# Kernel tuning notes

Measured on AMD Instinct MI355X. Metric: run time of the kernel, lower is better.

## Reference

```python
import jax, jax.numpy as jnp
import numpy as np

T, B, D, H, O = 128, 256, 512, 1024, 20
THR = 1.0
ALPHA = float(np.exp(-1.0 / 20.0))  # exp(-dt/tau_m)
KAPPA = float(np.exp(-1.0 / 20.0))  # exp(-dt/tau_o)
B_O = 0.0


def setup_inputs() -> dict:
    key = jax.random.key(0)
    k1, k2, k3, k4 = jax.random.split(key, 4)
    x = jax.random.normal(k1, (T, B, D), dtype=jnp.float32)
    # kaiming_normal: std = sqrt(2/fan_in), gain = 1.0
    w_in = jax.random.normal(k2, (H, D), dtype=jnp.float32) * np.sqrt(2.0 / D)
    w_rec = jax.random.normal(k3, (H, H), dtype=jnp.float32) * np.sqrt(2.0 / H)
    w_out = jax.random.normal(k4, (O, H), dtype=jnp.float32) * np.sqrt(2.0 / H)
    return {"x": x, "w_in": w_in, "w_rec": w_rec, "w_out": w_out}


def reference(x, w_in, w_rec, w_out):
    # mask out self-recurrence (diagonal zeroed)
    w_rec_eff = w_rec * (1.0 - jnp.eye(w_rec.shape[0], dtype=w_rec.dtype))

    def step(carry, x_t):
        v, z, vo = carry
        v_new = ALPHA * v + z @ w_rec_eff.T + x_t @ w_in.T - z * THR
        z_new = (v_new > THR).astype(v_new.dtype)
        vo_new = KAPPA * vo + z_new @ w_out.T + B_O
        return (v_new, z_new, vo_new), vo_new

    v0 = jnp.zeros((x.shape[1], w_rec.shape[0]), dtype=x.dtype)
    vo0 = jnp.zeros((x.shape[1], w_out.shape[0]), dtype=x.dtype)
    # torch loop runs t = 0..T-2, consuming x[0..T-2]; vo[0] stays zero
    _, vo_rest = jax.lax.scan(step, (v0, v0, vo0), x[:-1])
    vo = jnp.concatenate([vo0[None], vo_rest], axis=0)  # [T, B, O]
    return jax.nn.softmax(vo, axis=2)
```

## Files before the change

kernel.cpp:

```cpp
#include <hip/hip_runtime.h>
#include <math.h>


#define T_ 128
#define B_ 256
#define D_ 512
#define H_ 1024
#define O_ 20
#define ST_ 127
#define WPB 32
#define ALPHA_F ((float)0.95122942450071400909)
#define KAPPA_F ((float)0.95122942450071400909)

typedef float v2f __attribute__((ext_vector_type(2)));

#if defined(__has_builtin)
#if __has_builtin(__builtin_elementwise_fma)
#define PK_FMA(a, b, c) __builtin_elementwise_fma(a, b, c)
#endif
#if __has_builtin(__builtin_amdgcn_global_load_lds)
#define HAVE_GLL 1
#endif
#endif
#ifndef PK_FMA
static __device__ inline v2f pk_fma_impl(v2f a, v2f b, v2f c) {
    v2f r; r[0] = __fmaf_rn(a[0], b[0], c[0]); r[1] = __fmaf_rn(a[1], b[1], c[1]);
    return r;
}
#define PK_FMA(a, b, c) pk_fma_impl(a, b, c)
#endif

static __device__ __forceinline__ void f2acc(float2& a, const float2 b) {
    a.x = __fadd_rn(a.x, b.x);
    a.y = __fadd_rn(a.y, b.y);
}

static __device__ __forceinline__ unsigned spread16(unsigned x) {
    x &= 0xFFFFu;
    x = (x | (x << 8)) & 0x00FF00FFu;
    x = (x | (x << 4)) & 0x0F0F0F0Fu;
    x = (x | (x << 2)) & 0x33333333u;
    x = (x | (x << 1)) & 0x55555555u;
    return x;
}

__global__ __launch_bounds__(256) void transpose_k(
    const float* __restrict__ src, float* __restrict__ dst,
    int rows, int cols, int zero_diag)
{
    __shared__ float tile[32][33];
    const int c0 = blockIdx.x * 32;
    const int r0 = blockIdx.y * 32;
    const int tid = threadIdx.x;
    const int lr = tid >> 3;
    const int lc = (tid & 7) * 4;
    const float4 vv = *(const float4*)(src + (size_t)(r0 + lr) * cols + c0 + lc);
    tile[lr][lc+0] = vv.x; tile[lr][lc+1] = vv.y;
    tile[lr][lc+2] = vv.z; tile[lr][lc+3] = vv.w;
    __syncthreads();
    const int wc = lr;
    const int wr = lc;
    float4 o;
    o.x = tile[wr+0][wc]; o.y = tile[wr+1][wc];
    o.z = tile[wr+2][wc]; o.w = tile[wr+3][wc];
    if (zero_diag) {
        const int c = c0 + wc;
        if (c == r0 + wr + 0) o.x = 0.f;
        if (c == r0 + wr + 1) o.y = 0.f;
        if (c == r0 + wr + 2) o.z = 0.f;
        if (c == r0 + wr + 3) o.w = 0.f;
    }
    *(float4*)(dst + (size_t)(c0 + wc) * rows + r0 + wr) = o;
}

__global__ __launch_bounds__(256) void srnn_init(
    float* __restrict__ v, unsigned* __restrict__ z0)
{
    const int i = blockIdx.x * 256 + threadIdx.x;
    if (i < B_ * H_)  v[i]  = 0.0f;
    if (i < B_ * WPB) z0[i] = 0u;
}

#define SWC(r) ((((r) >> 3) & 3) << 2)
__global__ __launch_bounds__(256) void srnn_qsum(
    const float* __restrict__ x,
    const float* __restrict__ WinT,
    float* __restrict__ qs,
    int s0, int nsl)
{
    __shared__ float wt[32][68];
    __shared__ float xt[32][68];
    const int nwg = nsl * 64;
    const int rb  = (int)blockIdx.x;
    const int lb  = (rb & 7) * (nwg >> 3) + (rb >> 3);
    const int sl = lb >> 6;
    const int t = lb & 63;
    const int h0 = (t & 15) << 6;
    const int b0 = (t >> 4) << 6;
    const int tid = threadIdx.x;
    const int tx4 = (tid & 15) << 2;
    const int ty4 = (tid >> 4) << 2;
    const float* xs = x + (size_t)(s0 + sl) * (B_ * D_);

    const int idxa = tid * 2, idxb = tid * 2 + 1;
    const int wra = idxa >> 4, wca = (idxa & 15) << 2;
    const int wrb = idxb >> 4, wcb = (idxb & 15) << 2;
    const int bra = idxa >> 3, kqa = (idxa & 7) << 2;
    const int brb = idxb >> 3, kqb = (idxb & 7) << 2;

    v2f accA[4][2], accB[4][2];
    #pragma unroll
    for (int i = 0; i < 4; ++i) {
        accA[i][0]=(v2f)0.f; accA[i][1]=(v2f)0.f;
        accB[i][0]=(v2f)0.f; accB[i][1]=(v2f)0.f;
    }

    float4 wp0, wp1, xp0, xp1;
    auto qload = [&](int kc) {
        wp0 = *(const float4*)(WinT + (size_t)(kc*32 + wra)*H_ + h0 + wca);
        wp1 = *(const float4*)(WinT + (size_t)(kc*32 + wrb)*H_ + h0 + wcb);
        xp0 = *(const float4*)(xs + (size_t)(b0+bra)*D_ + kc*32 + kqa);
        xp1 = *(const float4*)(xs + (size_t)(b0+brb)*D_ + kc*32 + kqb);
    };
    auto qstore = [&]() {
        *(float4*)&wt[wra][wca] = wp0;
        *(float4*)&wt[wrb][wcb] = wp1;
        xt[kqa+0][bra ^ SWC(kqa+0)]=xp0.x; xt[kqa+1][bra ^ SWC(kqa+1)]=xp0.y;
        xt[kqa+2][bra ^ SWC(kqa+2)]=xp0.z; xt[kqa+3][bra ^ SWC(kqa+3)]=xp0.w;
        xt[kqb+0][brb ^ SWC(kqb+0)]=xp1.x; xt[kqb+1][brb ^ SWC(kqb+1)]=xp1.y;
        xt[kqb+2][brb ^ SWC(kqb+2)]=xp1.z; xt[kqb+3][brb ^ SWC(kqb+3)]=xp1.w;
    };
    auto qinner = [&](v2f (&ACC)[4][2]) {
        #pragma unroll
        for (int kk = 0; kk < 32; ++kk) {
            const float4 zf = *(const float4*)&xt[kk][ty4 ^ SWC(kk)];
            const float4 wf = *(const float4*)&wt[kk][tx4];
            v2f wlo, whi;
            wlo[0]=wf.x; wlo[1]=wf.y; whi[0]=wf.z; whi[1]=wf.w;
            const float zz[4] = {zf.x, zf.y, zf.z, zf.w};
            #pragma unroll
            for (int i = 0; i < 4; ++i) {
                v2f zv; zv[0]=zz[i]; zv[1]=zz[i];
                ACC[i][0] = PK_FMA(zv, wlo, ACC[i][0]);
                ACC[i][1] = PK_FMA(zv, whi, ACC[i][1]);
            }
        }
    };

    qload(0);
    for (int kc = 0; kc < 10; ++kc) {
        __syncthreads();
        qstore();
        __syncthreads();
        qload(kc + 1);
        qinner(accA);
    }
    for (int kc = 10; kc < 16; ++kc) {
        __syncthreads();
        qstore();
        __syncthreads();
        if (kc < 15) qload(kc + 1);
        qinner(accB);
    }

    float* qd = qs + (size_t)sl * (B_ * H_);
    #pragma unroll
    for (int i = 0; i < 4; ++i) {
        float4 o;
        o.x = __fadd_rn(accA[i][0][0], accB[i][0][0]);
        o.y = __fadd_rn(accA[i][0][1], accB[i][0][1]);
        o.z = __fadd_rn(accA[i][1][0], accB[i][1][0]);
        o.w = __fadd_rn(accA[i][1][1], accB[i][1][1]);
        *(float4*)(qd + (size_t)(b0 + ty4 + i) * H_ + h0 + tx4) = o;
    }
}

#define STG_FLOATS (32 * 128)

static __device__ __forceinline__ void issue_stage(
    const float* __restrict__ WrecT, float (*wt)[STG_FLOATS],
    int s, int cb, int ht, int w, int tid)
{
#ifdef HAVE_GLL
    #pragma unroll
    for (int i = 0; i < 2; ++i) {
        const int row = s * 32 + i * 16 + (tid >> 5);
        const float* gs = WrecT + (size_t)row * H_ + ht * 128 + ((tid & 31) << 2);
        float* ld = &wt[cb][i * 2048 + w * 256];
        __builtin_amdgcn_global_load_lds(
            (const __attribute__((address_space(1))) void*)gs,
            (__attribute__((address_space(3))) void*)ld, 16, 0, 0);
    }
#else
    #pragma unroll
    for (int i = 0; i < 2; ++i) {
        const int row = s * 32 + i * 16 + (tid >> 5);
        const float4 tv = *(const float4*)(WrecT + (size_t)row * H_ + ht * 128 + ((tid & 31) << 2));
        *(float4*)&wt[cb][i * 2048 + tid * 4] = tv;
    }
#endif
}

#ifdef HAVE_GLL
#define WAITV2() asm volatile("s_waitcnt vmcnt(2)" ::: "memory")
#define WAITV0() asm volatile("s_waitcnt vmcnt(0)" ::: "memory")
#define STEPBAR() __builtin_amdgcn_s_barrier()
#else
#define WAITV2()
#define WAITV0()
#define STEPBAR() __syncthreads()
#endif

#define PROC_STAGE(SS, ACC) do { \
    const int n_ = __builtin_amdgcn_readfirstlane(__shfl((int)myc, (SS), 64)); \
    const unsigned short* kl_ = &klist2[SS][w][0]; \
    const char* wb_ = ((const char*)&wt[(SS) % 3][0]) + (ln << 3); \
    int i_ = 0; \
    for (; i_ + 8 <= n_; i_ += 8) { \
        const uint4 kk_ = *(const uint4*)(kl_ + i_); \
        const float2 r0_ = *(const float2*)(wb_ + (kk_.x & 0xFFFFu)); \
        const float2 r1_ = *(const float2*)(wb_ + (kk_.x >> 16)); \
        const float2 r2_ = *(const float2*)(wb_ + (kk_.y & 0xFFFFu)); \
        const float2 r3_ = *(const float2*)(wb_ + (kk_.y >> 16)); \
        const float2 r4_ = *(const float2*)(wb_ + (kk_.z & 0xFFFFu)); \
        const float2 r5_ = *(const float2*)(wb_ + (kk_.z >> 16)); \
        const float2 r6_ = *(const float2*)(wb_ + (kk_.w & 0xFFFFu)); \
        const float2 r7_ = *(const float2*)(wb_ + (kk_.w >> 16)); \
        f2acc(ACC, r0_); f2acc(ACC, r1_); f2acc(ACC, r2_); f2acc(ACC, r3_); \
        f2acc(ACC, r4_); f2acc(ACC, r5_); f2acc(ACC, r6_); f2acc(ACC, r7_); \
    } \
    if (i_ + 4 <= n_) { \
        const uint2 kk_ = *(const uint2*)(kl_ + i_); \
        const float2 r0_ = *(const float2*)(wb_ + (kk_.x & 0xFFFFu)); \
        const float2 r1_ = *(const float2*)(wb_ + (kk_.x >> 16)); \
        const float2 r2_ = *(const float2*)(wb_ + (kk_.y & 0xFFFFu)); \
        const float2 r3_ = *(const float2*)(wb_ + (kk_.y >> 16)); \
        f2acc(ACC, r0_); f2acc(ACC, r1_); f2acc(ACC, r2_); f2acc(ACC, r3_); \
        i_ += 4; \
    } \
    for (; i_ < n_; ++i_) { \
        const float2 r_ = *(const float2*)(wb_ + kl_[i_]); \
        f2acc(ACC, r_); \
    } \
} while (0)

#define STEP_S(SS, ACC) do { \
    if ((SS) < 31) { WAITV2(); } else { WAITV0(); } \
    STEPBAR(); \
    asm volatile("" ::: "memory"); \
    if ((SS) < 30) issue_stage(WrecT, wt, (SS) + 2, ((SS) + 2) % 3, ht, w, tid); \
    PROC_STAGE(SS, ACC); \
    asm volatile("" ::: "memory"); \
} while (0)

__global__ __launch_bounds__(512) void srnn_step(
    const float* __restrict__ WrecT,
    const float* __restrict__ qsum_s,
    const unsigned* __restrict__ zin,
    unsigned* __restrict__ zout,
    float* __restrict__ v)
{
    __shared__ float wt[3][STG_FLOATS];
    __shared__ unsigned short klist2[32][8][32];

    const int bid = (int)blockIdx.x;
    const int ht = bid & 7;
    const int bg = bid >> 3;
    const int tid = threadIdx.x;
    const int w = tid >> 6;
    const int ln = tid & 63;
    const int b = bg * 8 + w;

    unsigned zword = 0u;
    if (ln < 32) zword = zin[(size_t)b * WPB + ln];

    issue_stage(WrecT, wt, 0, 0, ht, w, tid);
    issue_stage(WrecT, wt, 1, 1, ht, w, tid);

    const int myc = __popc(zword);
    if (ln < 32) {
        unsigned short* kd = &klist2[ln][w][0];
        int ofs = 0;
        unsigned tw = zword;
        while (tw) {
            const int j = __builtin_ctz(tw);
            tw &= tw - 1;
            kd[ofs++] = (unsigned short)((unsigned)j << 9);
        }
    }

    float2 acc0 = {0.f, 0.f}, acc1 = {0.f, 0.f};
    float2 acc2 = {0.f, 0.f}, acc3 = {0.f, 0.f};

    STEP_S(0, acc0);  STEP_S(1, acc0);  STEP_S(2, acc0);  STEP_S(3, acc0);  STEP_S(4, acc0);
    STEP_S(5, acc0);  STEP_S(6, acc0);  STEP_S(7, acc0);  STEP_S(8, acc0);  STEP_S(9, acc0);
    STEP_S(10, acc1); STEP_S(11, acc1); STEP_S(12, acc1); STEP_S(13, acc1); STEP_S(14, acc1);
    STEP_S(15, acc1); STEP_S(16, acc1); STEP_S(17, acc1); STEP_S(18, acc1); STEP_S(19, acc1);
    STEP_S(20, acc2); STEP_S(21, acc2); STEP_S(22, acc2); STEP_S(23, acc2); STEP_S(24, acc2);
    STEP_S(25, acc2); STEP_S(26, acc2); STEP_S(27, acc2); STEP_S(28, acc2); STEP_S(29, acc2);
    STEP_S(30, acc3); STEP_S(31, acc3);

    const int h0 = ht * 128 + ln * 2;
    const size_t bh = (size_t)b * H_ + h0;
    const float2 qv = *(const float2*)(qsum_s + bh);
    const float2 vv = *(const float2*)(v + bh);
    const unsigned zwrd = (unsigned)__shfl((int)zword, ht * 4 + (ln >> 4), 64);
    const int bb0 = (ln & 15) * 2;

    const float a0c[2] = {acc0.x, acc0.y};
    const float a1c[2] = {acc1.x, acc1.y};
    const float a2c[2] = {acc2.x, acc2.y};
    const float a3c[2] = {acc3.x, acc3.y};
    const float qc[2]  = {qv.x, qv.y};
    const float vc[2]  = {vv.x, vv.y};

    float vn2[2];
    #pragma unroll
    for (int m = 0; m < 2; ++m) {
        const float P  = __fadd_rn(__fadd_rn(__fadd_rn(a0c[m], a1c[m]), a2c[m]), a3c[m]);
        const float zs = ((zwrd >> (bb0 + m)) & 1u) ? 1.f : 0.f;
        const float t1 = __fmul_rn(ALPHA_F, vc[m]);
        const float t2 = __fadd_rn(t1, P);
        const float t3 = __fadd_rn(t2, qc[m]);
        vn2[m] = __fsub_rn(t3, zs);
    }
    float2 vst; vst.x = vn2[0]; vst.y = vn2[1];
    *(float2*)(v + bh) = vst;

    const unsigned long long bx = __ballot(vn2[0] > 1.0f);
    const unsigned long long by = __ballot(vn2[1] > 1.0f);
    if (ln < 4) {
        const unsigned ex = (unsigned)((bx >> (ln * 16)) & 0xFFFFull);
        const unsigned ey = (unsigned)((by >> (ln * 16)) & 0xFFFFull);
        const unsigned word = spread16(ex) | (spread16(ey) << 1);
        zout[(size_t)b * WPB + ht * 4 + ln] = word;
    }
}

__global__ __launch_bounds__(256) void srnn_zo(
    const unsigned* __restrict__ zhist,
    const float* __restrict__ w_out,
    float* __restrict__ zo)
{
    __shared__ float red[16][16][O_ + 1];
    const int s  = blockIdx.x >> 4;
    const int bg = blockIdx.x & 15;
    const int tid = threadIdx.x;
    const int bl  = tid >> 4;
    const int seg = tid & 15;
    const int b = bg * 16 + bl;
    const unsigned* zr = zhist + ((size_t)s * B_ + b) * WPB;
    const unsigned w0 = zr[seg * 2 + 0];
    const unsigned w1 = zr[seg * 2 + 1];

    float a[O_];
    #pragma unroll
    for (int o = 0; o < O_; ++o) a[o] = 0.f;
    const int hb = seg * 64;
    for (int j = 0; j < 32; ++j) {
        if ((w0 >> j) & 1u) {
            #pragma unroll
            for (int o = 0; o < O_; ++o) a[o] += w_out[(size_t)o * H_ + hb + j];
        }
    }
    for (int j = 0; j < 32; ++j) {
        if ((w1 >> j) & 1u) {
            #pragma unroll
            for (int o = 0; o < O_; ++o) a[o] += w_out[(size_t)o * H_ + hb + 32 + j];
        }
    }
    #pragma unroll
    for (int o = 0; o < O_; ++o) red[bl][seg][o] = a[o];
    __syncthreads();
    for (int ww = tid; ww < 16 * O_; ww += 256) {
        const int bl2 = ww / O_, o = ww % O_;
        float sum = 0.f;
        #pragma unroll
        for (int g = 0; g < 16; ++g) sum += red[bl2][g][o];
        zo[((size_t)s * B_ + bg * 16 + bl2) * O_ + o] = sum;
    }
}

__global__ __launch_bounds__(64) void srnn_scan(
    const float* __restrict__ zo,
    float* __restrict__ out)
{
    __shared__ float vos[T_][O_];
    const int b = blockIdx.x;
    const int tid = threadIdx.x;
    if (tid < O_) {
        float vo = 0.f;
        vos[0][tid] = 0.f;
        for (int sp = 0; sp < ST_; ++sp) {
            vo = KAPPA_F * vo + zo[((size_t)sp * B_ + b) * O_ + tid];
            vos[sp + 1][tid] = vo;
        }
    }
    __syncthreads();
    for (int t = tid; t < T_; t += 64) {
        float m = -1e30f;
        #pragma unroll
        for (int o = 0; o < O_; ++o) m = fmaxf(m, vos[t][o]);
        float e[O_];
        float ssum = 0.f;
        #pragma unroll
        for (int o = 0; o < O_; ++o) {
            const float ee = expf(vos[t][o] - m);
            e[o] = ee;
            ssum += ee;
        }
        const float inv = 1.f / ssum;
        #pragma unroll
        for (int o = 0; o < O_; ++o)
            out[((size_t)t * B_ + b) * O_ + o] = e[o] * inv;
    }
}

extern "C" void kernel_launch(void* const* d_in, const int* in_sizes, int n_in,
                              void* d_out, int out_size, void* d_ws, size_t ws_size,
                              hipStream_t stream) {
    const float* x     = (const float*)d_in[0];
    const float* w_in  = (const float*)d_in[1];
    const float* w_rec = (const float*)d_in[2];
    const float* w_out = (const float*)d_in[3];
    float* out = (float*)d_out;

    float*    WrecT = (float*)d_ws;
    float*    WinT  = WrecT + (size_t)H_ * H_;
    float*    v     = WinT  + (size_t)D_ * H_;
    unsigned* z0    = (unsigned*)(v + (size_t)B_ * H_);
    unsigned* zhist = z0 + (size_t)B_ * WPB;
    float*    zo    = (float*)(zhist + (size_t)ST_ * B_ * WPB);
    float*    qbuf  = zo + (size_t)ST_ * B_ * O_;

    const size_t used = (size_t)((char*)qbuf - (char*)d_ws);
    const size_t qstep = (size_t)B_ * H_ * sizeof(float);
    size_t avail = (ws_size > used) ? (ws_size - used) : 0;
    int G = (int)(avail / qstep);
    if (G < 1)  G = 1;
    if (G > ST_) G = ST_;

    transpose_k<<<dim3(32, 32), 256, 0, stream>>>(w_rec, WrecT, H_, H_, 1);
    transpose_k<<<dim3(16, 32), 256, 0, stream>>>(w_in,  WinT,  H_, D_, 0);
    srnn_init<<<(B_ * H_ + 255) / 256, 256, 0, stream>>>(v, z0);

    const unsigned* zprev = z0;
    for (int s0 = 0; s0 < ST_; s0 += G) {
        const int gc = (ST_ - s0 < G) ? (ST_ - s0) : G;
        srnn_qsum<<<gc * 64, 256, 0, stream>>>(x, WinT, qbuf, s0, gc);
        for (int sl = 0; sl < gc; ++sl) {
            const int s = s0 + sl;
            unsigned* zcur = zhist + (size_t)s * B_ * WPB;
            srnn_step<<<256, 512, 0, stream>>>(
                WrecT, qbuf + (size_t)sl * B_ * H_, zprev, zcur, v);
            zprev = zcur;
        }
    }

    srnn_zo<<<ST_ * 16, 256, 0, stream>>>(zhist, w_out, zo);
    srnn_scan<<<B_, 64, 0, stream>>>(zo, out);
}
```

Measured before the change: 3.038 ms.

## Stage recurrent weights in 128-row chunks with double buffering and merged spike lists

Moves the recurrent-weight staging from 32 stages of 32 rows (triple-buffered, one barrier per stage) to 8 stages of 128 rows (double-buffered, 64 KB each). Spike index lists for four 32-row words are merged into one list per stage using prefix offsets, so the gather loop runs longer with fewer remainder iterations. The goal is to cut the number of barriers and the per-stage loop overhead. In exchange it uses much more LDS (128 KB), which can limit occupancy, and it waits on vmcnt(0) each stage, leaving less room for prefetch overlap. The four accumulator splits are kept by splitting stages 2 and 7 at the word-10 and word-30 boundaries.

```diff
diff --git a/kernel.cpp b/kernel.cpp
--- a/kernel.cpp
+++ b/kernel.cpp
@@ -175,83 +175,39 @@
     }
 }
 
-#define STG_FLOATS (32 * 128)
-
-static __device__ __forceinline__ void issue_stage(
-    const float* __restrict__ WrecT, float (*wt)[STG_FLOATS],
-    int s, int cb, int ht, int w, int tid)
+#define STG_FLOATS (128 * 128)
+
+static __device__ __forceinline__ void issue_stage8(
+    const float* __restrict__ WrecT, float* buf,
+    int s, int ht, int w, int tid)
 {
 #ifdef HAVE_GLL
     #pragma unroll
-    for (int i = 0; i < 2; ++i) {
-        const int row = s * 32 + i * 16 + (tid >> 5);
+    for (int i = 0; i < 8; ++i) {
+        const int row = s * 128 + i * 16 + (tid >> 5);
         const float* gs = WrecT + (size_t)row * H_ + ht * 128 + ((tid & 31) << 2);
-        float* ld = &wt[cb][i * 2048 + w * 256];
+        float* ld = buf + (i * 16 + 2 * w) * 128;
         __builtin_amdgcn_global_load_lds(
             (const __attribute__((address_space(1))) void*)gs,
             (__attribute__((address_space(3))) void*)ld, 16, 0, 0);
     }
 #else
     #pragma unroll
-    for (int i = 0; i < 2; ++i) {
-        const int row = s * 32 + i * 16 + (tid >> 5);
+    for (int i = 0; i < 8; ++i) {
+        const int row = s * 128 + i * 16 + (tid >> 5);
         const float4 tv = *(const float4*)(WrecT + (size_t)row * H_ + ht * 128 + ((tid & 31) << 2));
-        *(float4*)&wt[cb][i * 2048 + tid * 4] = tv;
+        *(float4*)&buf[(i * 16 + (tid >> 5)) * 128 + ((tid & 31) << 2)] = tv;
     }
 #endif
 }
 
 #ifdef HAVE_GLL
-#define WAITV2() asm volatile("s_waitcnt vmcnt(2)" ::: "memory")
 #define WAITV0() asm volatile("s_waitcnt vmcnt(0)" ::: "memory")
 #define STEPBAR() __builtin_amdgcn_s_barrier()
 #else
-#define WAITV2()
 #define WAITV0()
 #define STEPBAR() __syncthreads()
 #endif
-
-#define PROC_STAGE(SS, ACC) do { \
-    const int n_ = __builtin_amdgcn_readfirstlane(__shfl((int)myc, (SS), 64)); \
-    const unsigned short* kl_ = &klist2[SS][w][0]; \
-    const char* wb_ = ((const char*)&wt[(SS) % 3][0]) + (ln << 3); \
-    int i_ = 0; \
-    for (; i_ + 8 <= n_; i_ += 8) { \
-        const uint4 kk_ = *(const uint4*)(kl_ + i_); \
-        const float2 r0_ = *(const float2*)(wb_ + (kk_.x & 0xFFFFu)); \
-        const float2 r1_ = *(const float2*)(wb_ + (kk_.x >> 16)); \
-        const float2 r2_ = *(const float2*)(wb_ + (kk_.y & 0xFFFFu)); \
-        const float2 r3_ = *(const float2*)(wb_ + (kk_.y >> 16)); \
-        const float2 r4_ = *(const float2*)(wb_ + (kk_.z & 0xFFFFu)); \
-        const float2 r5_ = *(const float2*)(wb_ + (kk_.z >> 16)); \
-        const float2 r6_ = *(const float2*)(wb_ + (kk_.w & 0xFFFFu)); \
-        const float2 r7_ = *(const float2*)(wb_ + (kk_.w >> 16)); \
-        f2acc(ACC, r0_); f2acc(ACC, r1_); f2acc(ACC, r2_); f2acc(ACC, r3_); \
-        f2acc(ACC, r4_); f2acc(ACC, r5_); f2acc(ACC, r6_); f2acc(ACC, r7_); \
-    } \
-    if (i_ + 4 <= n_) { \
-        const uint2 kk_ = *(const uint2*)(kl_ + i_); \
-        const float2 r0_ = *(const float2*)(wb_ + (kk_.x & 0xFFFFu)); \
-        const float2 r1_ = *(const float2*)(wb_ + (kk_.x >> 16)); \
-        const float2 r2_ = *(const float2*)(wb_ + (kk_.y & 0xFFFFu)); \
-        const float2 r3_ = *(const float2*)(wb_ + (kk_.y >> 16)); \
-        f2acc(ACC, r0_); f2acc(ACC, r1_); f2acc(ACC, r2_); f2acc(ACC, r3_); \
-        i_ += 4; \
-    } \
-    for (; i_ < n_; ++i_) { \
-        const float2 r_ = *(const float2*)(wb_ + kl_[i_]); \
-        f2acc(ACC, r_); \
-    } \
-} while (0)
-
-#define STEP_S(SS, ACC) do { \
-    if ((SS) < 31) { WAITV2(); } else { WAITV0(); } \
-    STEPBAR(); \
-    asm volatile("" ::: "memory"); \
-    if ((SS) < 30) issue_stage(WrecT, wt, (SS) + 2, ((SS) + 2) % 3, ht, w, tid); \
-    PROC_STAGE(SS, ACC); \
-    asm volatile("" ::: "memory"); \
-} while (0)
 
 __global__ __launch_bounds__(512) void srnn_step(
     const float* __restrict__ WrecT,
@@ -260,8 +216,8 @@
     unsigned* __restrict__ zout,
     float* __restrict__ v)
 {
-    __shared__ float wt[3][STG_FLOATS];
-    __shared__ unsigned short klist2[32][8][32];
+    __shared__ float wt[2][STG_FLOATS];
+    __shared__ unsigned short klist[8][8][128];
 
     const int bid = (int)blockIdx.x;
     const int ht = bid & 7;
@@ -274,31 +230,100 @@
     unsigned zword = 0u;
     if (ln < 32) zword = zin[(size_t)b * WPB + ln];
 
-    issue_stage(WrecT, wt, 0, 0, ht, w, tid);
-    issue_stage(WrecT, wt, 1, 1, ht, w, tid);
+    issue_stage8(WrecT, &wt[0][0], 0, ht, w, tid);
 
     const int myc = __popc(zword);
+    const int gbase = ln & ~3;
+    const int p0 = __shfl(myc, gbase | 0, 64);
+    const int p1 = __shfl(myc, gbase | 1, 64);
+    const int p2 = __shfl(myc, gbase | 2, 64);
+    const int q = ln & 3;
+    const int pre = (q > 0 ? p0 : 0) + (q > 1 ? p1 : 0) + (q > 2 ? p2 : 0);
+    const int tot = pre + myc;
     if (ln < 32) {
-        unsigned short* kd = &klist2[ln][w][0];
+        unsigned short* kd = &klist[ln >> 2][w][pre];
+        const unsigned base = (unsigned)(q << 14);
         int ofs = 0;
         unsigned tw = zword;
         while (tw) {
             const int j = __builtin_ctz(tw);
             tw &= tw - 1;
-            kd[ofs++] = (unsigned short)((unsigned)j << 9);
-        }
-    }
+            kd[ofs++] = (unsigned short)(base + ((unsigned)j << 9));
+        }
+    }
+
+    const int n0 = __builtin_amdgcn_readfirstlane(__shfl(tot, 3,  64));
+    const int n1 = __builtin_amdgcn_readfirstlane(__shfl(tot, 7,  64));
+    const int n2 = __builtin_amdgcn_readfirstlane(__shfl(tot, 11, 64));
+    const int n3 = __builtin_amdgcn_readfirstlane(__shfl(tot, 15, 64));
+    const int n4 = __builtin_amdgcn_readfirstlane(__shfl(tot, 19, 64));
+    const int n5 = __builtin_amdgcn_readfirstlane(__shfl(tot, 23, 64));
+    const int n6 = __builtin_amdgcn_readfirstlane(__shfl(tot, 27, 64));
+    const int n7 = __builtin_amdgcn_readfirstlane(__shfl(tot, 31, 64));
+    const int sp2 = __builtin_amdgcn_readfirstlane(__shfl(pre, 10, 64));
+    const int sp7 = __builtin_amdgcn_readfirstlane(__shfl(pre, 30, 64));
 
     float2 acc0 = {0.f, 0.f}, acc1 = {0.f, 0.f};
     float2 acc2 = {0.f, 0.f}, acc3 = {0.f, 0.f};
 
-    STEP_S(0, acc0);  STEP_S(1, acc0);  STEP_S(2, acc0);  STEP_S(3, acc0);  STEP_S(4, acc0);
-    STEP_S(5, acc0);  STEP_S(6, acc0);  STEP_S(7, acc0);  STEP_S(8, acc0);  STEP_S(9, acc0);
-    STEP_S(10, acc1); STEP_S(11, acc1); STEP_S(12, acc1); STEP_S(13, acc1); STEP_S(14, acc1);
-    STEP_S(15, acc1); STEP_S(16, acc1); STEP_S(17, acc1); STEP_S(18, acc1); STEP_S(19, acc1);
-    STEP_S(20, acc2); STEP_S(21, acc2); STEP_S(22, acc2); STEP_S(23, acc2); STEP_S(24, acc2);
-    STEP_S(25, acc2); STEP_S(26, acc2); STEP_S(27, acc2); STEP_S(28, acc2); STEP_S(29, acc2);
-    STEP_S(30, acc3); STEP_S(31, acc3);
+    auto proc = [&](float2& ACC, const unsigned short* kl_, const char* wb_,
+                    int lo, int hi) {
+        int i_ = lo;
+        while (i_ < hi && (i_ & 7)) {
+            const float2 r_ = *(const float2*)(wb_ + kl_[i_]);
+            f2acc(ACC, r_);
+            ++i_;
+        }
+        for (; i_ + 8 <= hi; i_ += 8) {
+            const uint4 kk_ = *(const uint4*)(kl_ + i_);
+            const float2 r0_ = *(const float2*)(wb_ + (kk_.x & 0xFFFFu));
+            const float2 r1_ = *(const float2*)(wb_ + (kk_.x >> 16));
+            const float2 r2_ = *(const float2*)(wb_ + (kk_.y & 0xFFFFu));
+            const float2 r3_ = *(const float2*)(wb_ + (kk_.y >> 16));
+            const float2 r4_ = *(const float2*)(wb_ + (kk_.z & 0xFFFFu));
+            const float2 r5_ = *(const float2*)(wb_ + (kk_.z >> 16));
+            const float2 r6_ = *(const float2*)(wb_ + (kk_.w & 0xFFFFu));
+            const float2 r7_ = *(const float2*)(wb_ + (kk_.w >> 16));
+            f2acc(ACC, r0_); f2acc(ACC, r1_); f2acc(ACC, r2_); f2acc(ACC, r3_);
+            f2acc(ACC, r4_); f2acc(ACC, r5_); f2acc(ACC, r6_); f2acc(ACC, r7_);
+        }
+        if (i_ + 4 <= hi) {
+            const uint2 kk_ = *(const uint2*)(kl_ + i_);
+            const float2 r0_ = *(const float2*)(wb_ + (kk_.x & 0xFFFFu));
+            const float2 r1_ = *(const float2*)(wb_ + (kk_.x >> 16));
+            const float2 r2_ = *(const float2*)(wb_ + (kk_.y & 0xFFFFu));
+            const float2 r3_ = *(const float2*)(wb_ + (kk_.y >> 16));
+            f2acc(ACC, r0_); f2acc(ACC, r1_); f2acc(ACC, r2_); f2acc(ACC, r3_);
+            i_ += 4;
+        }
+        for (; i_ < hi; ++i_) {
+            const float2 r_ = *(const float2*)(wb_ + kl_[i_]);
+            f2acc(ACC, r_);
+        }
+    };
+
+#define WB(SS) (((const char*)&wt[(SS) & 1][0]) + (ln << 3))
+#define KL(SS) (&klist[SS][w][0])
+#define STEP_HEAD(SS) do { \
+    WAITV0(); \
+    STEPBAR(); \
+    asm volatile("" ::: "memory"); \
+    if ((SS) < 7) issue_stage8(WrecT, &wt[((SS) + 1) & 1][0], (SS) + 1, ht, w, tid); \
+} while (0)
+
+    STEP_HEAD(0); proc(acc0, KL(0), WB(0), 0, n0);
+    STEP_HEAD(1); proc(acc0, KL(1), WB(1), 0, n1);
+    STEP_HEAD(2); proc(acc0, KL(2), WB(2), 0, sp2);
+                  proc(acc1, KL(2), WB(2), sp2, n2);
+    STEP_HEAD(3); proc(acc1, KL(3), WB(3), 0, n3);
+    STEP_HEAD(4); proc(acc1, KL(4), WB(4), 0, n4);
+    STEP_HEAD(5); proc(acc2, KL(5), WB(5), 0, n5);
+    STEP_HEAD(6); proc(acc2, KL(6), WB(6), 0, n6);
+    STEP_HEAD(7); proc(acc2, KL(7), WB(7), 0, sp7);
+                  proc(acc3, KL(7), WB(7), sp7, n7);
+#undef WB
+#undef KL
+#undef STEP_HEAD
 
     const int h0 = ht * 128 + ln * 2;
     const size_t bh = (size_t)b * H_ + h0;
```

After: 2.502 ms. -17.6%, faster.
